# Optimization experiments

Hardware: AMD Instinct MI355X
Metric: run time of the kernel (lower is better)

Reference implementation:

```python
import jax, jax.numpy as jnp
import numpy as np

C = 128          # channels
L = 2            # num_layers
NA = 30000       # nodes of type 'a'
NB = 30000       # nodes of type 'b'
E = 150000       # edges per edge type
SEED_SIZE = 1024
EPS = 1e-5


def _ln(x, g, b):
    # LayerNorm over last dim (biased variance, eps=1e-5), matches nn.LayerNorm / PyG LayerNorm(mode='node')
    m = x.mean(-1, keepdims=True)
    v = ((x - m) ** 2).mean(-1, keepdims=True)
    return (x - m) * jax.lax.rsqrt(v + EPS) * g + b


def _seg_mean(msg, dst, n):
    # PyG aggr='mean': mean of incoming messages, 0 for isolated nodes
    s = jax.ops.segment_sum(msg, dst, num_segments=n)
    cnt = jax.ops.segment_sum(jnp.ones((dst.shape[0],), msg.dtype), dst, num_segments=n)
    return s / jnp.maximum(cnt, 1.0)[:, None]


def _prmp_conv(x_src, x_dst, edge, w1, b1, w2, b2, g, be, uw, ub):
    src, dst = edge[0], edge[1]
    xi = x_dst[dst]                                   # [E, C] dst feats per edge
    xj = x_src[src]                                   # [E, C] src feats per edge
    h = jax.nn.relu(jax.lax.stop_gradient(xi) @ w1 + b1)  # pred_mlp on detached x_i
    pred = h @ w2 + b2
    msg = _ln(xj - pred, g, be)                       # LayerNorm(residual) per edge
    agg = _seg_mean(msg, dst, x_dst.shape[0])         # mean aggregation to dst nodes
    return jax.nn.relu(jnp.concatenate([x_dst, agg], -1) @ uw + ub)  # update_mlp


def setup_inputs() -> dict:
    key = jax.random.key(0)
    ks = jax.random.split(key, 12)
    edge_ab = jnp.stack([jax.random.randint(ks[2], (E,), 0, NA, jnp.int32),
                         jax.random.randint(ks[3], (E,), 0, NB, jnp.int32)])
    edge_ba = jnp.stack([jax.random.randint(ks[4], (E,), 0, NB, jnp.int32),
                         jax.random.randint(ks[5], (E,), 0, NA, jnp.int32)])
    return {
        "x_a": jax.random.normal(ks[0], (NA, C), jnp.float32),
        "x_b": jax.random.normal(ks[1], (NB, C), jnp.float32),
        "edge_ab": edge_ab,
        "edge_ba": edge_ba,
        "pred_w1": jax.random.normal(ks[6], (L, 2, C, C), jnp.float32) * 0.05,
        "pred_b1": jnp.zeros((L, 2, C), jnp.float32),
        "pred_w2": jax.random.normal(ks[7], (L, 2, C, C), jnp.float32) * 0.05,
        "pred_b2": jnp.zeros((L, 2, C), jnp.float32),
        "msg_gamma": jnp.ones((L, 2, C), jnp.float32),
        "msg_beta": jnp.zeros((L, 2, C), jnp.float32),
        "upd_w": jax.random.normal(ks[8], (L, 2, 2 * C, C), jnp.float32) * 0.05,
        "upd_b": jnp.zeros((L, 2, C), jnp.float32),
        "node_gamma": jnp.ones((L, 2, C), jnp.float32),
        "node_beta": jnp.zeros((L, 2, C), jnp.float32),
        "head_w": jax.random.normal(ks[9], (C, 1), jnp.float32) * 0.05,
        "head_b": jnp.zeros((1,), jnp.float32),
        "seed_size": SEED_SIZE,
    }


def reference(x_a, x_b, edge_ab, edge_ba, pred_w1, pred_b1, pred_w2, pred_b2,
              msg_gamma, msg_beta, upd_w, upd_b, node_gamma, node_beta,
              head_w, head_b, seed_size):
    enc = lambda t: jnp.nan_to_num(t, nan=0.0, posinf=1.0, neginf=-1.0)
    x_a, x_b = enc(x_a), enc(x_b)
    for l in range(L):
        # edge type 0: a -> b ; edge type 1: b -> a (HeteroConv aggr='sum' is trivial: one conv per dst type)
        nb = _prmp_conv(x_a, x_b, edge_ab, pred_w1[l, 0], pred_b1[l, 0], pred_w2[l, 0], pred_b2[l, 0],
                        msg_gamma[l, 0], msg_beta[l, 0], upd_w[l, 0], upd_b[l, 0])
        na = _prmp_conv(x_b, x_a, edge_ba, pred_w1[l, 1], pred_b1[l, 1], pred_w2[l, 1], pred_b2[l, 1],
                        msg_gamma[l, 1], msg_beta[l, 1], upd_w[l, 1], upd_b[l, 1])
        na = jnp.nan_to_num(na, nan=0.0, posinf=10.0, neginf=-10.0)
        nb = jnp.nan_to_num(nb, nan=0.0, posinf=10.0, neginf=-10.0)
        x_a = jax.nn.relu(_ln(na, node_gamma[l, 0], node_beta[l, 0]))
        x_b = jax.nn.relu(_ln(nb, node_gamma[l, 1], node_beta[l, 1]))
    # head: single Linear(C -> 1) on the seed nodes of the entity table (type 'a')
    return x_a[:seed_size] @ head_w + head_b
```

## Files before the change

kernel.cpp:

```cpp
#include <hip/hip_runtime.h>

#define CC 128
#define SCAN_T 1024
#define SCAN_I 4

typedef __attribute__((ext_vector_type(8))) short bf16x8;
typedef __attribute__((ext_vector_type(4))) float f32x4;
#define MFMA16(a, b, c) __builtin_amdgcn_mfma_f32_16x16x32_bf16(a, b, c, 0, 0, 0)

__device__ __forceinline__ float enc_nan(float v) {
    if (v != v) return 0.f;
    if (v > 3.0e38f) return 1.f;
    if (v < -3.0e38f) return -1.f;
    return v;
}

__device__ __forceinline__ ushort f2bf(float x) {
    unsigned u = __builtin_bit_cast(unsigned, x);
    u += 0x7fff + ((u >> 16) & 1);
    return (ushort)(u >> 16);
}
__device__ __forceinline__ float bf2f(ushort h) {
    return __builtin_bit_cast(float, ((unsigned)h) << 16);
}

__device__ __forceinline__ int swz128(int row, int k) { return (row * 128 + k) ^ ((row & 7) << 3); }
__device__ __forceinline__ int swz256(int row, int k) { return (row * 256 + k) ^ ((row & 7) << 3); }

__global__ __launch_bounds__(256)
void k_init(const float* __restrict__ xin, ushort* __restrict__ xbf,
            float2* __restrict__ stat, int N)
{
    int row = blockIdx.x * 8 + (threadIdx.x >> 5);
    int s = threadIdx.x & 31;
    if (row >= N) return;
    float4 v = *reinterpret_cast<const float4*>(xin + (size_t)row * CC + s * 4);
    ushort h0 = f2bf(enc_nan(v.x)), h1 = f2bf(enc_nan(v.y));
    ushort h2 = f2bf(enc_nan(v.z)), h3 = f2bf(enc_nan(v.w));
    ushort4 hv = make_ushort4(h0, h1, h2, h3);
    *reinterpret_cast<ushort4*>(xbf + (size_t)row * CC + s * 4) = hv;
    float r0 = bf2f(h0), r1 = bf2f(h1), r2 = bf2f(h2), r3 = bf2f(h3);
    float sm = (r0 + r1) + (r2 + r3);
    float sq = fmaf(r0, r0, fmaf(r1, r1, fmaf(r2, r2, r3 * r3)));
    #pragma unroll
    for (int m = 1; m < 32; m <<= 1) { sm += __shfl_xor(sm, m); sq += __shfl_xor(sq, m); }
    if (s == 0) stat[row] = make_float2(sm, sq);
}

__global__ __launch_bounds__(256)
void k_wcvt(const float* __restrict__ pw1, const float* __restrict__ pw2,
            const float* __restrict__ uw,
            ushort* __restrict__ w1t, ushort* __restrict__ w2t, ushort* __restrict__ uwt)
{
    int i = blockIdx.x * 256 + threadIdx.x;
    int t = i >> 16;
    int r = i & 65535;
    if (r < 16384) {
        int k = r >> 7, c = r & 127;
        w1t[(size_t)t * 16384 + c * 128 + k] = f2bf(pw1[(size_t)t * 16384 + k * 128 + c]);
    } else if (r < 32768) {
        int rr = r - 16384;
        int k = rr >> 7, c = rr & 127;
        w2t[(size_t)t * 16384 + c * 128 + k] = f2bf(pw2[(size_t)t * 16384 + k * 128 + c]);
    } else {
        int rr = r - 32768;
        int k = rr >> 7, c = rr & 127;
        uwt[(size_t)t * 32768 + c * 256 + k] = f2bf(uw[(size_t)t * 32768 + k * 128 + c]);
    }
}

__global__ __launch_bounds__(256)
void k_hist_dual(const int* __restrict__ dst_b, int Eab, int* __restrict__ cnt_b,
                 const int* __restrict__ dst_a, int Eba, int* __restrict__ cnt_a)
{
    int i = blockIdx.x * 256 + threadIdx.x;
    if (i < Eab) atomicAdd(&cnt_b[dst_b[i]], 1);
    else if (i - Eab < Eba) atomicAdd(&cnt_a[dst_a[i - Eab]], 1);
}

__global__ __launch_bounds__(SCAN_T)
void k_scan_dual(const int* __restrict__ cnt0, int* __restrict__ rowp0, int* __restrict__ off0, int n0,
                 const int* __restrict__ cnt1, int* __restrict__ rowp1, int* __restrict__ off1, int n1)
{
    const int* cnt = (blockIdx.x == 0) ? cnt0 : cnt1;
    int* row_ptr   = (blockIdx.x == 0) ? rowp0 : rowp1;
    int* off       = (blockIdx.x == 0) ? off0 : off1;
    int n          = (blockIdx.x == 0) ? n0 : n1;

    __shared__ int wsum[SCAN_T / 64];
    __shared__ int carry_s;
    const int tid = threadIdx.x, lane = tid & 63, wid = tid >> 6;
    if (tid == 0) carry_s = 0;
    __syncthreads();
    const int chunk = SCAN_T * SCAN_I;
    for (int base = 0; base < n; base += chunk) {
        int i0 = base + tid * SCAN_I;
        int v[SCAN_I];
        int local = 0;
        #pragma unroll
        for (int t = 0; t < SCAN_I; ++t) {
            int i = i0 + t;
            v[t] = (i < n) ? cnt[i] : 0;
            local += v[t];
        }
        int incl = local;
        #pragma unroll
        for (int d = 1; d < 64; d <<= 1) {
            int t = __shfl_up(incl, d);
            if (lane >= d) incl += t;
        }
        if (lane == 63) wsum[wid] = incl;
        __syncthreads();
        if (wid == 0) {
            int wv = (lane < SCAN_T / 64) ? wsum[lane] : 0;
            int winc = wv;
            #pragma unroll
            for (int d = 1; d < SCAN_T / 64; d <<= 1) {
                int t = __shfl_up(winc, d);
                if (lane >= d) winc += t;
            }
            if (lane < SCAN_T / 64) wsum[lane] = winc - wv;
        }
        __syncthreads();
        int carry = carry_s;
        int excl = carry + wsum[wid] + incl - local;
        #pragma unroll
        for (int t = 0; t < SCAN_I; ++t) {
            int i = i0 + t;
            if (i < n) { row_ptr[i] = excl; off[i] = excl; }
            excl += v[t];
        }
        __syncthreads();
        if (tid == SCAN_T - 1) carry_s = carry + wsum[SCAN_T / 64 - 1] + incl;
        __syncthreads();
    }
    if (threadIdx.x == 0) row_ptr[n] = carry_s;
}

__global__ __launch_bounds__(256)
void k_scatter_dual(const int* __restrict__ src_b, const int* __restrict__ dst_b, int Eab,
                    int* __restrict__ off_b, int* __restrict__ srcs_ab,
                    const int* __restrict__ src_a, const int* __restrict__ dst_a, int Eba,
                    int* __restrict__ off_a, int* __restrict__ srcs_ba)
{
    int i = blockIdx.x * 256 + threadIdx.x;
    if (i < Eab) {
        int p = atomicAdd(&off_b[dst_b[i]], 1);
        srcs_ab[p] = src_b[i];
    } else if (i - Eab < Eba) {
        int j = i - Eab;
        int p = atomicAdd(&off_a[dst_a[j]], 1);
        srcs_ba[p] = src_a[j];
    }
}

__device__ __forceinline__ void pred_body(
    ushort* As, ushort* Hs,
    const ushort* __restrict__ xbf, ushort* __restrict__ pred_bf, int N, int blk,
    const ushort* __restrict__ w1t, const float* __restrict__ b1,
    const ushort* __restrict__ w2t, const float* __restrict__ b2)
{
    const int tid = threadIdx.x;
    const int base = blk * 32;

    {
        int row = tid >> 3, k0 = (tid & 7) << 4;
        int node = base + row;
        bf16x8 v0 = {}, v1 = {};
        if (node < N) {
            v0 = *reinterpret_cast<const bf16x8*>(xbf + (size_t)node * CC + k0);
            v1 = *reinterpret_cast<const bf16x8*>(xbf + (size_t)node * CC + k0 + 8);
        }
        *reinterpret_cast<bf16x8*>(&As[swz128(row, k0)])     = v0;
        *reinterpret_cast<bf16x8*>(&As[swz128(row, k0 + 8)]) = v1;
    }
    __syncthreads();

    const int w = tid >> 6, l = tid & 63;
    const int lr = l & 15, lg = l >> 4;

    f32x4 acc[2][2] = {};
    for (int kb = 0; kb < 4; ++kb) {
        int k = kb * 32 + lg * 8;
        bf16x8 a0 = *reinterpret_cast<const bf16x8*>(&As[swz128(lr, k)]);
        bf16x8 a1 = *reinterpret_cast<const bf16x8*>(&As[swz128(lr + 16, k)]);
        bf16x8 b0 = *reinterpret_cast<const bf16x8*>(&w1t[(size_t)(w * 32 + lr) * 128 + k]);
        bf16x8 b1v = *reinterpret_cast<const bf16x8*>(&w1t[(size_t)(w * 32 + 16 + lr) * 128 + k]);
        acc[0][0] = MFMA16(a0, b0, acc[0][0]);
        acc[0][1] = MFMA16(a0, b1v, acc[0][1]);
        acc[1][0] = MFMA16(a1, b0, acc[1][0]);
        acc[1][1] = MFMA16(a1, b1v, acc[1][1]);
    }
    {
        float bc[2] = { b1[w * 32 + lr], b1[w * 32 + 16 + lr] };
        #pragma unroll
        for (int mi = 0; mi < 2; ++mi)
            #pragma unroll
            for (int ni = 0; ni < 2; ++ni) {
                int col = w * 32 + ni * 16 + lr;
                #pragma unroll
                for (int j = 0; j < 4; ++j) {
                    int row = mi * 16 + lg * 4 + j;
                    Hs[swz128(row, col)] = f2bf(fmaxf(acc[mi][ni][j] + bc[ni], 0.f));
                }
            }
    }
    __syncthreads();

    f32x4 acc2[2][2] = {};
    for (int kb = 0; kb < 4; ++kb) {
        int k = kb * 32 + lg * 8;
        bf16x8 a0 = *reinterpret_cast<const bf16x8*>(&Hs[swz128(lr, k)]);
        bf16x8 a1 = *reinterpret_cast<const bf16x8*>(&Hs[swz128(lr + 16, k)]);
        bf16x8 b0 = *reinterpret_cast<const bf16x8*>(&w2t[(size_t)(w * 32 + lr) * 128 + k]);
        bf16x8 b1v = *reinterpret_cast<const bf16x8*>(&w2t[(size_t)(w * 32 + 16 + lr) * 128 + k]);
        acc2[0][0] = MFMA16(a0, b0, acc2[0][0]);
        acc2[0][1] = MFMA16(a0, b1v, acc2[0][1]);
        acc2[1][0] = MFMA16(a1, b0, acc2[1][0]);
        acc2[1][1] = MFMA16(a1, b1v, acc2[1][1]);
    }
    {
        float bc[2] = { b2[w * 32 + lr], b2[w * 32 + 16 + lr] };
        #pragma unroll
        for (int mi = 0; mi < 2; ++mi)
            #pragma unroll
            for (int ni = 0; ni < 2; ++ni) {
                int col = w * 32 + ni * 16 + lr;
                #pragma unroll
                for (int j = 0; j < 4; ++j) {
                    int row = mi * 16 + lg * 4 + j;
                    int node = base + row;
                    if (node < N)
                        pred_bf[(size_t)node * CC + col] = f2bf(acc2[mi][ni][j] + bc[ni]);
                }
            }
    }
}

__global__ __launch_bounds__(256)
void k_pred_dual(const ushort* __restrict__ xb, ushort* __restrict__ prd_b, int NB, int GB,
                 const ushort* __restrict__ w1t0, const float* __restrict__ b10,
                 const ushort* __restrict__ w2t0, const float* __restrict__ b20,
                 const ushort* __restrict__ xa, ushort* __restrict__ prd_a, int NA,
                 const ushort* __restrict__ w1t1, const float* __restrict__ b11,
                 const ushort* __restrict__ w2t1, const float* __restrict__ b21)
{
    __shared__ __align__(16) ushort As[32 * 128];
    __shared__ __align__(16) ushort Hs[32 * 128];
    if ((int)blockIdx.x < GB)
        pred_body(As, Hs, xb, prd_b, NB, blockIdx.x, w1t0, b10, w2t0, b20);
    else
        pred_body(As, Hs, xa, prd_a, NA, blockIdx.x - GB, w1t1, b11, w2t1, b21);
}

__device__ __forceinline__ void agg_body(
    const int* __restrict__ rowp, const int* __restrict__ srcs,
    const ushort* __restrict__ xsrc, const float2* __restrict__ statx,
    const ushort* __restrict__ pred_bf, const float* __restrict__ g,
    const float* __restrict__ be, ushort* __restrict__ agg_bf, int N, int blk)
{
    const int wid = threadIdx.x >> 6;
    const int lane = threadIdx.x & 63;
    const int d = blk * 4 + wid;
    if (d >= N) return;
    const int quarter = lane >> 4;
    const int c = (lane & 15) * 8;
    const int jb = rowp[d], je = rowp[d + 1];
    const int deg = je - jb;

    bf16x8 prb = *reinterpret_cast<const bf16x8*>(pred_bf + (size_t)d * CC + c);
    float pr[8];
    #pragma unroll
    for (int i = 0; i < 8; ++i) pr[i] = bf2f((ushort)prb[i]);

    float sp = 0.f, qp = 0.f;
    #pragma unroll
    for (int i = 0; i < 8; ++i) { sp += pr[i]; qp = fmaf(pr[i], pr[i], qp); }
    #pragma unroll
    for (int m = 1; m < 16; m <<= 1) { sp += __shfl_xor(sp, m); qp += __shfl_xor(qp, m); }

    float a[8] = {};
    float rsum = 0.f, cmsum = 0.f;
    for (int j = jb + quarter; j < je; j += 4) {
        const int sidx = srcs[j];
        bf16x8 xb_ = *reinterpret_cast<const bf16x8*>(xsrc + (size_t)sidx * CC + c);
        const float2 st = statx[sidx];
        float xj[8];
        #pragma unroll
        for (int i = 0; i < 8; ++i) xj[i] = bf2f((ushort)xb_[i]);
        float dot = 0.f;
        #pragma unroll
        for (int i = 0; i < 8; ++i) dot = fmaf(xj[i], pr[i], dot);
        #pragma unroll
        for (int m = 1; m < 16; m <<= 1) dot += __shfl_xor(dot, m);
        const float mean = (st.x - sp) * (1.f / 128.f);
        const float var = fmaf(-2.f, dot, st.y + qp) * (1.f / 128.f) - mean * mean;
        const float r = rsqrtf(var + 1e-5f);
        rsum += r;
        cmsum = fmaf(mean, r, cmsum);
        #pragma unroll
        for (int i = 0; i < 8; ++i) a[i] = fmaf(xj[i], r, a[i]);
    }
    #pragma unroll
    for (int i = 0; i < 8; ++i) { a[i] += __shfl_xor(a[i], 16); a[i] += __shfl_xor(a[i], 32); }
    rsum += __shfl_xor(rsum, 16);  rsum += __shfl_xor(rsum, 32);
    cmsum += __shfl_xor(cmsum, 16); cmsum += __shfl_xor(cmsum, 32);

    if (quarter == 0) {
        ushort o8[8];
        if (deg > 0) {
            const float inv = 1.f / (float)deg;
            const float4 g0 = *reinterpret_cast<const float4*>(g + c);
            const float4 g1 = *reinterpret_cast<const float4*>(g + c + 4);
            const float4 b0 = *reinterpret_cast<const float4*>(be + c);
            const float4 b1 = *reinterpret_cast<const float4*>(be + c + 4);
            const float gv[8] = { g0.x, g0.y, g0.z, g0.w, g1.x, g1.y, g1.z, g1.w };
            const float bv[8] = { b0.x, b0.y, b0.z, b0.w, b1.x, b1.y, b1.z, b1.w };
            #pragma unroll
            for (int i = 0; i < 8; ++i)
                o8[i] = f2bf(fmaf((a[i] - pr[i] * rsum - cmsum) * inv, gv[i], bv[i]));
        } else {
            #pragma unroll
            for (int i = 0; i < 8; ++i) o8[i] = 0;
        }
        *reinterpret_cast<bf16x8*>(agg_bf + (size_t)d * CC + c) =
            *reinterpret_cast<bf16x8*>(&o8[0]);
    }
}

__global__ __launch_bounds__(256)
void k_agg_dual(const int* __restrict__ rowp_b, const int* __restrict__ srcs_ab,
                const ushort* __restrict__ xa, const float2* __restrict__ stat_a,
                const ushort* __restrict__ prd_b, const float* __restrict__ g0,
                const float* __restrict__ be0, ushort* __restrict__ agg_b, int NB, int GBa,
                const int* __restrict__ rowp_a, const int* __restrict__ srcs_ba,
                const ushort* __restrict__ xb, const float2* __restrict__ stat_b,
                const ushort* __restrict__ prd_a, const float* __restrict__ g1,
                const float* __restrict__ be1, ushort* __restrict__ agg_a, int NA)
{
    if ((int)blockIdx.x < GBa)
        agg_body(rowp_b, srcs_ab, xa, stat_a, prd_b, g0, be0, agg_b, NB, blockIdx.x);
    else
        agg_body(rowp_a, srcs_ba, xb, stat_b, prd_a, g1, be1, agg_a, NA, blockIdx.x - GBa);
}

__device__ __forceinline__ void update_body(
    ushort* As, float (*os)[CC + 4],
    const ushort* __restrict__ xbf, const ushort* __restrict__ agg_bf,
    ushort* __restrict__ xout, float2* __restrict__ statOut, int N, int blk,
    const ushort* __restrict__ uwt, const float* __restrict__ ub,
    const float* __restrict__ ng, const float* __restrict__ nb,
    const float* __restrict__ hw, const float* __restrict__ hb,
    float* __restrict__ hout, int headS)
{
    const int tid = threadIdx.x;
    const int base = blk * 32;

    {
        int row = tid >> 3, k0 = (tid & 7) << 4;
        int node = base + row;
        bf16x8 v0 = {}, v1 = {}, v2 = {}, v3 = {};
        if (node < N) {
            v0 = *reinterpret_cast<const bf16x8*>(xbf + (size_t)node * CC + k0);
            v1 = *reinterpret_cast<const bf16x8*>(xbf + (size_t)node * CC + k0 + 8);
            v2 = *reinterpret_cast<const bf16x8*>(agg_bf + (size_t)node * CC + k0);
            v3 = *reinterpret_cast<const bf16x8*>(agg_bf + (size_t)node * CC + k0 + 8);
        }
        *reinterpret_cast<bf16x8*>(&As[swz256(row, k0)])           = v0;
        *reinterpret_cast<bf16x8*>(&As[swz256(row, k0 + 8)])       = v1;
        *reinterpret_cast<bf16x8*>(&As[swz256(row, 128 + k0)])     = v2;
        *reinterpret_cast<bf16x8*>(&As[swz256(row, 128 + k0 + 8)]) = v3;
    }
    __syncthreads();

    const int w = tid >> 6, l = tid & 63;
    const int lr = l & 15, lg = l >> 4;

    f32x4 acc[2][2] = {};
    for (int kb = 0; kb < 8; ++kb) {
        int k = kb * 32 + lg * 8;
        bf16x8 a0 = *reinterpret_cast<const bf16x8*>(&As[swz256(lr, k)]);
        bf16x8 a1 = *reinterpret_cast<const bf16x8*>(&As[swz256(lr + 16, k)]);
        bf16x8 b0 = *reinterpret_cast<const bf16x8*>(&uwt[(size_t)(w * 32 + lr) * 256 + k]);
        bf16x8 b1v = *reinterpret_cast<const bf16x8*>(&uwt[(size_t)(w * 32 + 16 + lr) * 256 + k]);
        acc[0][0] = MFMA16(a0, b0, acc[0][0]);
        acc[0][1] = MFMA16(a0, b1v, acc[0][1]);
        acc[1][0] = MFMA16(a1, b0, acc[1][0]);
        acc[1][1] = MFMA16(a1, b1v, acc[1][1]);
    }
    {
        float bc[2] = { ub[w * 32 + lr], ub[w * 32 + 16 + lr] };
        #pragma unroll
        for (int mi = 0; mi < 2; ++mi)
            #pragma unroll
            for (int ni = 0; ni < 2; ++ni) {
                int col = w * 32 + ni * 16 + lr;
                #pragma unroll
                for (int j = 0; j < 4; ++j) {
                    int row = mi * 16 + lg * 4 + j;
                    os[row][col] = fmaxf(acc[mi][ni][j] + bc[ni], 0.f);
                }
            }
    }
    __syncthreads();

    const int lane = tid & 63;
    const int nl = (tid >> 6) * 8 + (lane >> 3);
    const int cl = lane & 7;
    float vals[16];
    float sm = 0.f, sq = 0.f;
    #pragma unroll
    for (int t = 0; t < 16; ++t) {
        float u = os[nl][cl + 8 * t];
        vals[t] = u; sm += u; sq = fmaf(u, u, sq);
    }
    #pragma unroll
    for (int m = 1; m < 8; m <<= 1) { sm += __shfl_xor(sm, m); sq += __shfl_xor(sq, m); }
    float mean = sm * (1.f / 128.f);
    float var = sq * (1.f / 128.f) - mean * mean;
    float r = rsqrtf(var + 1e-5f);
    int node = base + nl;
    if (node < N) {
        float so = 0.f, sqo = 0.f, hsum = 0.f;
        bool doHead = (node < headS);
        #pragma unroll
        for (int t = 0; t < 16; ++t) {
            int cch = cl + 8 * t;
            float o = fmaxf(fmaf((vals[t] - mean) * r, ng[cch], nb[cch]), 0.f);
            ushort ob = f2bf(o);
            xout[(size_t)node * CC + cch] = ob;
            float orr = bf2f(ob);
            so += orr; sqo = fmaf(orr, orr, sqo);
            if (doHead) hsum = fmaf(o, hw[cch], hsum);
        }
        #pragma unroll
        for (int m = 1; m < 8; m <<= 1) { so += __shfl_xor(so, m); sqo += __shfl_xor(sqo, m); }
        if (doHead) {
            #pragma unroll
            for (int m = 1; m < 8; m <<= 1) hsum += __shfl_xor(hsum, m);
            if (cl == 0) hout[node] = hsum + hb[0];
        }
        if (cl == 0) statOut[node] = make_float2(so, sqo);
    }
}

__global__ __launch_bounds__(256)
void k_update_dual(const ushort* __restrict__ xb, const ushort* __restrict__ agg_b,
                   ushort* __restrict__ xb_o, float2* __restrict__ stat_b, int NB, int GB,
                   const ushort* __restrict__ uwt0, const float* __restrict__ ub0,
                   const float* __restrict__ ng0, const float* __restrict__ nb0,
                   const ushort* __restrict__ xa, const ushort* __restrict__ agg_a,
                   ushort* __restrict__ xa_o, float2* __restrict__ stat_a, int NA,
                   const ushort* __restrict__ uwt1, const float* __restrict__ ub1,
                   const float* __restrict__ ng1, const float* __restrict__ nb1,
                   const float* __restrict__ hw, const float* __restrict__ hb,
                   float* __restrict__ hout, int headS)
{
    __shared__ __align__(16) ushort As[32 * 256];
    __shared__ float os[32][CC + 4];
    if ((int)blockIdx.x < GB)
        update_body(As, os, xb, agg_b, xb_o, stat_b, NB, blockIdx.x,
                    uwt0, ub0, ng0, nb0, hw, hb, hout, 0);
    else
        update_body(As, os, xa, agg_a, xa_o, stat_a, NA, blockIdx.x - GB,
                    uwt1, ub1, ng1, nb1, hw, hb, hout, headS);
}

extern "C" void kernel_launch(void* const* d_in, const int* in_sizes, int n_in,
                              void* d_out, int out_size, void* d_ws, size_t ws_size,
                              hipStream_t stream)
{
    const float* x_a_in = (const float*)d_in[0];
    const float* x_b_in = (const float*)d_in[1];
    const int*   e_ab   = (const int*)d_in[2];
    const int*   e_ba   = (const int*)d_in[3];
    const float* pw1    = (const float*)d_in[4];
    const float* pb1    = (const float*)d_in[5];
    const float* pw2    = (const float*)d_in[6];
    const float* pb2    = (const float*)d_in[7];
    const float* mgam   = (const float*)d_in[8];
    const float* mbet   = (const float*)d_in[9];
    const float* uw     = (const float*)d_in[10];
    const float* ubias  = (const float*)d_in[11];
    const float* ngam   = (const float*)d_in[12];
    const float* nbet   = (const float*)d_in[13];
    const float* hw     = (const float*)d_in[14];
    const float* hb     = (const float*)d_in[15];

    const int NA  = in_sizes[0] / CC;
    const int NB  = in_sizes[1] / CC;
    const int Eab = in_sizes[2] / 2;
    const int Eba = in_sizes[3] / 2;

    float* ws = (float*)d_ws;
    size_t off = 0;
    ushort* xa    = (ushort*)(ws + off); off += (size_t)NA * CC / 2;
    ushort* xb    = (ushort*)(ws + off); off += (size_t)NB * CC / 2;
    ushort* prd_b = (ushort*)(ws + off); off += (size_t)NB * CC / 2;
    ushort* prd_a = (ushort*)(ws + off); off += (size_t)NA * CC / 2;
    ushort* agg_a = (ushort*)(ws + off); off += (size_t)NA * CC / 2;
    ushort* agg_b = (ushort*)(ws + off); off += (size_t)NB * CC / 2;
    float2* stat_a = (float2*)(ws + off); off += (size_t)NA * 2;
    float2* stat_b = (float2*)(ws + off); off += (size_t)NB * 2;
    ushort* w1t  = (ushort*)(ws + off); off += 4 * 16384 / 2;
    ushort* w2t  = (ushort*)(ws + off); off += 4 * 16384 / 2;
    ushort* uwt  = (ushort*)(ws + off); off += 4 * 32768 / 2;
    int* iw = (int*)(ws + off);
    size_t ioff = 0;
    int* cnt_b   = iw + ioff; ioff += NB;
    int* cnt_a   = iw + ioff; ioff += NA;
    int* rowp_b  = iw + ioff; ioff += NB + 1;
    int* rowp_a  = iw + ioff; ioff += NA + 1;
    int* off_b   = iw + ioff; ioff += NB;
    int* off_a   = iw + ioff; ioff += NA;
    int* srcs_ab = iw + ioff; ioff += Eab;
    int* srcs_ba = iw + ioff; ioff += Eba;

    const int GB  = (NB + 31) / 32, GA = (NA + 31) / 32;
    const int GBa = (NB + 3) / 4,  GAa = (NA + 3) / 4;

    k_init<<<dim3((NA + 7) / 8), dim3(256), 0, stream>>>(x_a_in, xa, stat_a, NA);
    k_init<<<dim3((NB + 7) / 8), dim3(256), 0, stream>>>(x_b_in, xb, stat_b, NB);

    k_wcvt<<<dim3(1024), dim3(256), 0, stream>>>(pw1, pw2, uw, w1t, w2t, uwt);

    hipMemsetAsync(cnt_b, 0, (size_t)(NB + NA) * sizeof(int), stream);
    k_hist_dual<<<dim3((Eab + Eba + 255) / 256), dim3(256), 0, stream>>>(
        e_ab + Eab, Eab, cnt_b, e_ba + Eba, Eba, cnt_a);
    k_scan_dual<<<dim3(2), dim3(SCAN_T), 0, stream>>>(
        cnt_b, rowp_b, off_b, NB, cnt_a, rowp_a, off_a, NA);
    k_scatter_dual<<<dim3((Eab + Eba + 255) / 256), dim3(256), 0, stream>>>(
        e_ab, e_ab + Eab, Eab, off_b, srcs_ab,
        e_ba, e_ba + Eba, Eba, off_a, srcs_ba);

    for (int l = 0; l < 2; ++l) {
        int t0 = l * 2 + 0;
        int t1 = l * 2 + 1;
        int headS = (l == 1) ? out_size : 0;

        k_pred_dual<<<dim3(GB + GA), dim3(256), 0, stream>>>(
            xb, prd_b, NB, GB,
            w1t + (size_t)t0 * 16384, pb1 + t0 * CC, w2t + (size_t)t0 * 16384, pb2 + t0 * CC,
            xa, prd_a, NA,
            w1t + (size_t)t1 * 16384, pb1 + t1 * CC, w2t + (size_t)t1 * 16384, pb2 + t1 * CC);

        k_agg_dual<<<dim3(GBa + GAa), dim3(256), 0, stream>>>(
            rowp_b, srcs_ab, xa, stat_a, prd_b, mgam + t0 * CC, mbet + t0 * CC, agg_b, NB, GBa,
            rowp_a, srcs_ba, xb, stat_b, prd_a, mgam + t1 * CC, mbet + t1 * CC, agg_a, NA);

        k_update_dual<<<dim3(GB + GA), dim3(256), 0, stream>>>(
            xb, agg_b, xb, stat_b, NB, GB,
            uwt + (size_t)t0 * 32768, ubias + t0 * CC, ngam + t0 * CC, nbet + t0 * CC,
            xa, agg_a, xa, stat_a, NA,
            uwt + (size_t)t1 * 32768, ubias + t1 * CC, ngam + t1 * CC, nbet + t1 * CC,
            hw, hb, (float*)d_out, headS);
    }
}
```

Measured before the change: 241.1 us.

## Fuse prediction MLP, edge aggregation and update MLP into one per-layer kernel

Replaces the three per-layer kernels (pred, agg, update) with a single kernel in which each 32-node block computes the prediction MLP into shared memory, aggregates neighbour messages into shared memory, then runs the update MLP and node LayerNorm. Node features and stats are now double-buffered across layers, and the two init launches are merged into one. This removes the global round-trips of the pred and agg intermediates and two launches per layer. In exchange, the aggregation now runs with one wave per 8 nodes in sequence inside the fused block, which may reduce latency hiding for the irregular gathers.

```diff
diff --git a/kernel.cpp b/kernel.cpp
--- a/kernel.cpp
+++ b/kernel.cpp
@@ -25,26 +25,32 @@
 }
 
 __device__ __forceinline__ int swz128(int row, int k) { return (row * 128 + k) ^ ((row & 7) << 3); }
-__device__ __forceinline__ int swz256(int row, int k) { return (row * 256 + k) ^ ((row & 7) << 3); }
 
 __global__ __launch_bounds__(256)
-void k_init(const float* __restrict__ xin, ushort* __restrict__ xbf,
-            float2* __restrict__ stat, int N)
+void k_init_dual(const float* __restrict__ xa_in, ushort* __restrict__ xa,
+                 float2* __restrict__ stat_a, int NA,
+                 const float* __restrict__ xb_in, ushort* __restrict__ xb,
+                 float2* __restrict__ stat_b, int NB)
 {
     int row = blockIdx.x * 8 + (threadIdx.x >> 5);
     int s = threadIdx.x & 31;
-    if (row >= N) return;
+    const float* xin; ushort* xo; float2* st;
+    if (row < NA) { xin = xa_in; xo = xa; st = stat_a; }
+    else {
+        row -= NA;
+        if (row >= NB) return;
+        xin = xb_in; xo = xb; st = stat_b;
+    }
     float4 v = *reinterpret_cast<const float4*>(xin + (size_t)row * CC + s * 4);
     ushort h0 = f2bf(enc_nan(v.x)), h1 = f2bf(enc_nan(v.y));
     ushort h2 = f2bf(enc_nan(v.z)), h3 = f2bf(enc_nan(v.w));
-    ushort4 hv = make_ushort4(h0, h1, h2, h3);
-    *reinterpret_cast<ushort4*>(xbf + (size_t)row * CC + s * 4) = hv;
+    *reinterpret_cast<ushort4*>(xo + (size_t)row * CC + s * 4) = make_ushort4(h0, h1, h2, h3);
     float r0 = bf2f(h0), r1 = bf2f(h1), r2 = bf2f(h2), r3 = bf2f(h3);
     float sm = (r0 + r1) + (r2 + r3);
     float sq = fmaf(r0, r0, fmaf(r1, r1, fmaf(r2, r2, r3 * r3)));
     #pragma unroll
     for (int m = 1; m < 32; m <<= 1) { sm += __shfl_xor(sm, m); sq += __shfl_xor(sq, m); }
-    if (s == 0) stat[row] = make_float2(sm, sq);
+    if (s == 0) st[row] = make_float2(sm, sq);
 }
 
 __global__ __launch_bounds__(256)
@@ -154,12 +160,25 @@
     }
 }
 
-__device__ __forceinline__ void pred_body(
-    ushort* As, ushort* Hs,
-    const ushort* __restrict__ xbf, ushort* __restrict__ pred_bf, int N, int blk,
+__device__ __forceinline__ void layer_body(
+    char* smem,
+    const ushort* __restrict__ xdst, const ushort* __restrict__ xsrc,
+    const float2* __restrict__ stat_src,
+    const int* __restrict__ rowp, const int* __restrict__ srcs,
     const ushort* __restrict__ w1t, const float* __restrict__ b1,
-    const ushort* __restrict__ w2t, const float* __restrict__ b2)
-{
+    const ushort* __restrict__ w2t, const float* __restrict__ b2,
+    const float* __restrict__ mg, const float* __restrict__ mbt,
+    const ushort* __restrict__ uwt, const float* __restrict__ ub,
+    const float* __restrict__ ng, const float* __restrict__ nb,
+    ushort* __restrict__ xout, float2* __restrict__ statOut, int N, int blk,
+    const float* __restrict__ hw, const float* __restrict__ hb,
+    float* __restrict__ hout, int headS)
+{
+    ushort* As = (ushort*)smem;
+    ushort* Hs = (ushort*)(smem + 8192);
+    ushort* P  = (ushort*)(smem + 16384);
+    float (*os)[CC + 4] = (float(*)[CC + 4])(smem + 8192);
+
     const int tid = threadIdx.x;
     const int base = blk * 32;
 
@@ -168,8 +187,8 @@
         int node = base + row;
         bf16x8 v0 = {}, v1 = {};
         if (node < N) {
-            v0 = *reinterpret_cast<const bf16x8*>(xbf + (size_t)node * CC + k0);
-            v1 = *reinterpret_cast<const bf16x8*>(xbf + (size_t)node * CC + k0 + 8);
+            v0 = *reinterpret_cast<const bf16x8*>(xdst + (size_t)node * CC + k0);
+            v1 = *reinterpret_cast<const bf16x8*>(xdst + (size_t)node * CC + k0 + 8);
         }
         *reinterpret_cast<bf16x8*>(&As[swz128(row, k0)])     = v0;
         *reinterpret_cast<bf16x8*>(&As[swz128(row, k0 + 8)]) = v1;
@@ -179,19 +198,19 @@
     const int w = tid >> 6, l = tid & 63;
     const int lr = l & 15, lg = l >> 4;
 
-    f32x4 acc[2][2] = {};
-    for (int kb = 0; kb < 4; ++kb) {
-        int k = kb * 32 + lg * 8;
-        bf16x8 a0 = *reinterpret_cast<const bf16x8*>(&As[swz128(lr, k)]);
-        bf16x8 a1 = *reinterpret_cast<const bf16x8*>(&As[swz128(lr + 16, k)]);
-        bf16x8 b0 = *reinterpret_cast<const bf16x8*>(&w1t[(size_t)(w * 32 + lr) * 128 + k]);
-        bf16x8 b1v = *reinterpret_cast<const bf16x8*>(&w1t[(size_t)(w * 32 + 16 + lr) * 128 + k]);
-        acc[0][0] = MFMA16(a0, b0, acc[0][0]);
-        acc[0][1] = MFMA16(a0, b1v, acc[0][1]);
-        acc[1][0] = MFMA16(a1, b0, acc[1][0]);
-        acc[1][1] = MFMA16(a1, b1v, acc[1][1]);
-    }
     {
+        f32x4 acc[2][2] = {};
+        for (int kb = 0; kb < 4; ++kb) {
+            int k = kb * 32 + lg * 8;
+            bf16x8 a0 = *reinterpret_cast<const bf16x8*>(&As[swz128(lr, k)]);
+            bf16x8 a1 = *reinterpret_cast<const bf16x8*>(&As[swz128(lr + 16, k)]);
+            bf16x8 b0 = *reinterpret_cast<const bf16x8*>(&w1t[(size_t)(w * 32 + lr) * 128 + k]);
+            bf16x8 b1v = *reinterpret_cast<const bf16x8*>(&w1t[(size_t)(w * 32 + 16 + lr) * 128 + k]);
+            acc[0][0] = MFMA16(a0, b0, acc[0][0]);
+            acc[0][1] = MFMA16(a0, b1v, acc[0][1]);
+            acc[1][0] = MFMA16(a1, b0, acc[1][0]);
+            acc[1][1] = MFMA16(a1, b1v, acc[1][1]);
+        }
         float bc[2] = { b1[w * 32 + lr], b1[w * 32 + 16 + lr] };
         #pragma unroll
         for (int mi = 0; mi < 2; ++mi)
@@ -207,19 +226,19 @@
     }
     __syncthreads();
 
-    f32x4 acc2[2][2] = {};
-    for (int kb = 0; kb < 4; ++kb) {
-        int k = kb * 32 + lg * 8;
-        bf16x8 a0 = *reinterpret_cast<const bf16x8*>(&Hs[swz128(lr, k)]);
-        bf16x8 a1 = *reinterpret_cast<const bf16x8*>(&Hs[swz128(lr + 16, k)]);
-        bf16x8 b0 = *reinterpret_cast<const bf16x8*>(&w2t[(size_t)(w * 32 + lr) * 128 + k]);
-        bf16x8 b1v = *reinterpret_cast<const bf16x8*>(&w2t[(size_t)(w * 32 + 16 + lr) * 128 + k]);
-        acc2[0][0] = MFMA16(a0, b0, acc2[0][0]);
-        acc2[0][1] = MFMA16(a0, b1v, acc2[0][1]);
-        acc2[1][0] = MFMA16(a1, b0, acc2[1][0]);
-        acc2[1][1] = MFMA16(a1, b1v, acc2[1][1]);
-    }
     {
+        f32x4 acc[2][2] = {};
+        for (int kb = 0; kb < 4; ++kb) {
+            int k = kb * 32 + lg * 8;
+            bf16x8 a0 = *reinterpret_cast<const bf16x8*>(&Hs[swz128(lr, k)]);
+            bf16x8 a1 = *reinterpret_cast<const bf16x8*>(&Hs[swz128(lr + 16, k)]);
+            bf16x8 b0 = *reinterpret_cast<const bf16x8*>(&w2t[(size_t)(w * 32 + lr) * 128 + k]);
+            bf16x8 b1v = *reinterpret_cast<const bf16x8*>(&w2t[(size_t)(w * 32 + 16 + lr) * 128 + k]);
+            acc[0][0] = MFMA16(a0, b0, acc[0][0]);
+            acc[0][1] = MFMA16(a0, b1v, acc[0][1]);
+            acc[1][0] = MFMA16(a1, b0, acc[1][0]);
+            acc[1][1] = MFMA16(a1, b1v, acc[1][1]);
+        }
         float bc[2] = { b2[w * 32 + lr], b2[w * 32 + 16 + lr] };
         #pragma unroll
         for (int mi = 0; mi < 2; ++mi)
@@ -229,158 +248,86 @@
                 #pragma unroll
                 for (int j = 0; j < 4; ++j) {
                     int row = mi * 16 + lg * 4 + j;
-                    int node = base + row;
-                    if (node < N)
-                        pred_bf[(size_t)node * CC + col] = f2bf(acc2[mi][ni][j] + bc[ni]);
+                    P[row * CC + col] = f2bf(acc[mi][ni][j] + bc[ni]);
                 }
             }
     }
-}
-
-__global__ __launch_bounds__(256)
-void k_pred_dual(const ushort* __restrict__ xb, ushort* __restrict__ prd_b, int NB, int GB,
-                 const ushort* __restrict__ w1t0, const float* __restrict__ b10,
-                 const ushort* __restrict__ w2t0, const float* __restrict__ b20,
-                 const ushort* __restrict__ xa, ushort* __restrict__ prd_a, int NA,
-                 const ushort* __restrict__ w1t1, const float* __restrict__ b11,
-                 const ushort* __restrict__ w2t1, const float* __restrict__ b21)
-{
-    __shared__ __align__(16) ushort As[32 * 128];
-    __shared__ __align__(16) ushort Hs[32 * 128];
-    if ((int)blockIdx.x < GB)
-        pred_body(As, Hs, xb, prd_b, NB, blockIdx.x, w1t0, b10, w2t0, b20);
-    else
-        pred_body(As, Hs, xa, prd_a, NA, blockIdx.x - GB, w1t1, b11, w2t1, b21);
-}
-
-__device__ __forceinline__ void agg_body(
-    const int* __restrict__ rowp, const int* __restrict__ srcs,
-    const ushort* __restrict__ xsrc, const float2* __restrict__ statx,
-    const ushort* __restrict__ pred_bf, const float* __restrict__ g,
-    const float* __restrict__ be, ushort* __restrict__ agg_bf, int N, int blk)
-{
-    const int wid = threadIdx.x >> 6;
-    const int lane = threadIdx.x & 63;
-    const int d = blk * 4 + wid;
-    if (d >= N) return;
-    const int quarter = lane >> 4;
-    const int c = (lane & 15) * 8;
-    const int jb = rowp[d], je = rowp[d + 1];
-    const int deg = je - jb;
-
-    bf16x8 prb = *reinterpret_cast<const bf16x8*>(pred_bf + (size_t)d * CC + c);
-    float pr[8];
-    #pragma unroll
-    for (int i = 0; i < 8; ++i) pr[i] = bf2f((ushort)prb[i]);
-
-    float sp = 0.f, qp = 0.f;
-    #pragma unroll
-    for (int i = 0; i < 8; ++i) { sp += pr[i]; qp = fmaf(pr[i], pr[i], qp); }
-    #pragma unroll
-    for (int m = 1; m < 16; m <<= 1) { sp += __shfl_xor(sp, m); qp += __shfl_xor(qp, m); }
-
-    float a[8] = {};
-    float rsum = 0.f, cmsum = 0.f;
-    for (int j = jb + quarter; j < je; j += 4) {
-        const int sidx = srcs[j];
-        bf16x8 xb_ = *reinterpret_cast<const bf16x8*>(xsrc + (size_t)sidx * CC + c);
-        const float2 st = statx[sidx];
-        float xj[8];
-        #pragma unroll
-        for (int i = 0; i < 8; ++i) xj[i] = bf2f((ushort)xb_[i]);
-        float dot = 0.f;
-        #pragma unroll
-        for (int i = 0; i < 8; ++i) dot = fmaf(xj[i], pr[i], dot);
-        #pragma unroll
-        for (int m = 1; m < 16; m <<= 1) dot += __shfl_xor(dot, m);
-        const float mean = (st.x - sp) * (1.f / 128.f);
-        const float var = fmaf(-2.f, dot, st.y + qp) * (1.f / 128.f) - mean * mean;
-        const float r = rsqrtf(var + 1e-5f);
-        rsum += r;
-        cmsum = fmaf(mean, r, cmsum);
-        #pragma unroll
-        for (int i = 0; i < 8; ++i) a[i] = fmaf(xj[i], r, a[i]);
-    }
-    #pragma unroll
-    for (int i = 0; i < 8; ++i) { a[i] += __shfl_xor(a[i], 16); a[i] += __shfl_xor(a[i], 32); }
-    rsum += __shfl_xor(rsum, 16);  rsum += __shfl_xor(rsum, 32);
-    cmsum += __shfl_xor(cmsum, 16); cmsum += __shfl_xor(cmsum, 32);
-
-    if (quarter == 0) {
-        ushort o8[8];
-        if (deg > 0) {
-            const float inv = 1.f / (float)deg;
-            const float4 g0 = *reinterpret_cast<const float4*>(g + c);
-            const float4 g1 = *reinterpret_cast<const float4*>(g + c + 4);
-            const float4 b0 = *reinterpret_cast<const float4*>(be + c);
-            const float4 b1 = *reinterpret_cast<const float4*>(be + c + 4);
-            const float gv[8] = { g0.x, g0.y, g0.z, g0.w, g1.x, g1.y, g1.z, g1.w };
-            const float bv[8] = { b0.x, b0.y, b0.z, b0.w, b1.x, b1.y, b1.z, b1.w };
-            #pragma unroll
-            for (int i = 0; i < 8; ++i)
-                o8[i] = f2bf(fmaf((a[i] - pr[i] * rsum - cmsum) * inv, gv[i], bv[i]));
-        } else {
-            #pragma unroll
-            for (int i = 0; i < 8; ++i) o8[i] = 0;
-        }
-        *reinterpret_cast<bf16x8*>(agg_bf + (size_t)d * CC + c) =
-            *reinterpret_cast<bf16x8*>(&o8[0]);
-    }
-}
-
-__global__ __launch_bounds__(256)
-void k_agg_dual(const int* __restrict__ rowp_b, const int* __restrict__ srcs_ab,
-                const ushort* __restrict__ xa, const float2* __restrict__ stat_a,
-                const ushort* __restrict__ prd_b, const float* __restrict__ g0,
-                const float* __restrict__ be0, ushort* __restrict__ agg_b, int NB, int GBa,
-                const int* __restrict__ rowp_a, const int* __restrict__ srcs_ba,
-                const ushort* __restrict__ xb, const float2* __restrict__ stat_b,
-                const ushort* __restrict__ prd_a, const float* __restrict__ g1,
-                const float* __restrict__ be1, ushort* __restrict__ agg_a, int NA)
-{
-    if ((int)blockIdx.x < GBa)
-        agg_body(rowp_b, srcs_ab, xa, stat_a, prd_b, g0, be0, agg_b, NB, blockIdx.x);
-    else
-        agg_body(rowp_a, srcs_ba, xb, stat_b, prd_a, g1, be1, agg_a, NA, blockIdx.x - GBa);
-}
-
-__device__ __forceinline__ void update_body(
-    ushort* As, float (*os)[CC + 4],
-    const ushort* __restrict__ xbf, const ushort* __restrict__ agg_bf,
-    ushort* __restrict__ xout, float2* __restrict__ statOut, int N, int blk,
-    const ushort* __restrict__ uwt, const float* __restrict__ ub,
-    const float* __restrict__ ng, const float* __restrict__ nb,
-    const float* __restrict__ hw, const float* __restrict__ hb,
-    float* __restrict__ hout, int headS)
-{
-    const int tid = threadIdx.x;
-    const int base = blk * 32;
+    __syncthreads();
 
     {
-        int row = tid >> 3, k0 = (tid & 7) << 4;
-        int node = base + row;
-        bf16x8 v0 = {}, v1 = {}, v2 = {}, v3 = {};
-        if (node < N) {
-            v0 = *reinterpret_cast<const bf16x8*>(xbf + (size_t)node * CC + k0);
-            v1 = *reinterpret_cast<const bf16x8*>(xbf + (size_t)node * CC + k0 + 8);
-            v2 = *reinterpret_cast<const bf16x8*>(agg_bf + (size_t)node * CC + k0);
-            v3 = *reinterpret_cast<const bf16x8*>(agg_bf + (size_t)node * CC + k0 + 8);
-        }
-        *reinterpret_cast<bf16x8*>(&As[swz256(row, k0)])           = v0;
-        *reinterpret_cast<bf16x8*>(&As[swz256(row, k0 + 8)])       = v1;
-        *reinterpret_cast<bf16x8*>(&As[swz256(row, 128 + k0)])     = v2;
-        *reinterpret_cast<bf16x8*>(&As[swz256(row, 128 + k0 + 8)]) = v3;
-    }
-    __syncthreads();
-
-    const int w = tid >> 6, l = tid & 63;
-    const int lr = l & 15, lg = l >> 4;
+        const int quarter = l >> 4;
+        const int c = (l & 15) * 8;
+        const float4 g0 = *reinterpret_cast<const float4*>(mg + c);
+        const float4 g1 = *reinterpret_cast<const float4*>(mg + c + 4);
+        const float4 e0 = *reinterpret_cast<const float4*>(mbt + c);
+        const float4 e1 = *reinterpret_cast<const float4*>(mbt + c + 4);
+        const float gv[8] = { g0.x, g0.y, g0.z, g0.w, g1.x, g1.y, g1.z, g1.w };
+        const float bv[8] = { e0.x, e0.y, e0.z, e0.w, e1.x, e1.y, e1.z, e1.w };
+        for (int i = 0; i < 8; ++i) {
+            const int nl_ = w * 8 + i;
+            const int d = base + nl_;
+            if (d >= N) break;
+            bf16x8 prb = *reinterpret_cast<const bf16x8*>(&P[nl_ * CC + c]);
+            float pr[8];
+            #pragma unroll
+            for (int q = 0; q < 8; ++q) pr[q] = bf2f((ushort)prb[q]);
+            float sp = 0.f, qp = 0.f;
+            #pragma unroll
+            for (int q = 0; q < 8; ++q) { sp += pr[q]; qp = fmaf(pr[q], pr[q], qp); }
+            #pragma unroll
+            for (int m = 1; m < 16; m <<= 1) { sp += __shfl_xor(sp, m); qp += __shfl_xor(qp, m); }
+            const int jb = rowp[d], je = rowp[d + 1];
+            const int deg = je - jb;
+            float a[8] = {};
+            float rsum = 0.f, cmsum = 0.f;
+            for (int j = jb + quarter; j < je; j += 4) {
+                const int sidx = srcs[j];
+                bf16x8 xb_ = *reinterpret_cast<const bf16x8*>(xsrc + (size_t)sidx * CC + c);
+                const float2 st = stat_src[sidx];
+                float xj[8];
+                #pragma unroll
+                for (int q = 0; q < 8; ++q) xj[q] = bf2f((ushort)xb_[q]);
+                float dot = 0.f;
+                #pragma unroll
+                for (int q = 0; q < 8; ++q) dot = fmaf(xj[q], pr[q], dot);
+                #pragma unroll
+                for (int m = 1; m < 16; m <<= 1) dot += __shfl_xor(dot, m);
+                const float mean = (st.x - sp) * (1.f / 128.f);
+                const float var = fmaf(-2.f, dot, st.y + qp) * (1.f / 128.f) - mean * mean;
+                const float r = rsqrtf(var + 1e-5f);
+                rsum += r;
+                cmsum = fmaf(mean, r, cmsum);
+                #pragma unroll
+                for (int q = 0; q < 8; ++q) a[q] = fmaf(xj[q], r, a[q]);
+            }
+            #pragma unroll
+            for (int q = 0; q < 8; ++q) { a[q] += __shfl_xor(a[q], 16); a[q] += __shfl_xor(a[q], 32); }
+            rsum += __shfl_xor(rsum, 16);  rsum += __shfl_xor(rsum, 32);
+            cmsum += __shfl_xor(cmsum, 16); cmsum += __shfl_xor(cmsum, 32);
+            if (quarter == 0) {
+                ushort o8[8];
+                if (deg > 0) {
+                    const float inv = 1.f / (float)deg;
+                    #pragma unroll
+                    for (int q = 0; q < 8; ++q)
+                        o8[q] = f2bf(fmaf((a[q] - pr[q] * rsum - cmsum) * inv, gv[q], bv[q]));
+                } else {
+                    #pragma unroll
+                    for (int q = 0; q < 8; ++q) o8[q] = 0;
+                }
+                *reinterpret_cast<bf16x8*>(&Hs[swz128(nl_, c)]) = *reinterpret_cast<bf16x8*>(&o8[0]);
+            }
+        }
+    }
+    __syncthreads();
 
     f32x4 acc[2][2] = {};
     for (int kb = 0; kb < 8; ++kb) {
         int k = kb * 32 + lg * 8;
-        bf16x8 a0 = *reinterpret_cast<const bf16x8*>(&As[swz256(lr, k)]);
-        bf16x8 a1 = *reinterpret_cast<const bf16x8*>(&As[swz256(lr + 16, k)]);
+        const ushort* Ab = (k < 128) ? As : Hs;
+        int kl = k & 127;
+        bf16x8 a0 = *reinterpret_cast<const bf16x8*>(&Ab[swz128(lr, kl)]);
+        bf16x8 a1 = *reinterpret_cast<const bf16x8*>(&Ab[swz128(lr + 16, kl)]);
         bf16x8 b0 = *reinterpret_cast<const bf16x8*>(&uwt[(size_t)(w * 32 + lr) * 256 + k]);
         bf16x8 b1v = *reinterpret_cast<const bf16x8*>(&uwt[(size_t)(w * 32 + 16 + lr) * 256 + k]);
         acc[0][0] = MFMA16(a0, b0, acc[0][0]);
@@ -388,6 +335,8 @@
         acc[1][0] = MFMA16(a1, b0, acc[1][0]);
         acc[1][1] = MFMA16(a1, b1v, acc[1][1]);
     }
+    __syncthreads();
+
     {
         float bc[2] = { ub[w * 32 + lr], ub[w * 32 + 16 + lr] };
         #pragma unroll
@@ -404,9 +353,8 @@
     }
     __syncthreads();
 
-    const int lane = tid & 63;
-    const int nl = (tid >> 6) * 8 + (lane >> 3);
-    const int cl = lane & 7;
+    const int nl = w * 8 + (l >> 3);
+    const int cl = l & 7;
     float vals[16];
     float sm = 0.f, sq = 0.f;
     #pragma unroll
@@ -445,25 +393,36 @@
 }
 
 __global__ __launch_bounds__(256)
-void k_update_dual(const ushort* __restrict__ xb, const ushort* __restrict__ agg_b,
-                   ushort* __restrict__ xb_o, float2* __restrict__ stat_b, int NB, int GB,
-                   const ushort* __restrict__ uwt0, const float* __restrict__ ub0,
-                   const float* __restrict__ ng0, const float* __restrict__ nb0,
-                   const ushort* __restrict__ xa, const ushort* __restrict__ agg_a,
-                   ushort* __restrict__ xa_o, float2* __restrict__ stat_a, int NA,
-                   const ushort* __restrict__ uwt1, const float* __restrict__ ub1,
-                   const float* __restrict__ ng1, const float* __restrict__ nb1,
-                   const float* __restrict__ hw, const float* __restrict__ hb,
-                   float* __restrict__ hout, int headS)
-{
-    __shared__ __align__(16) ushort As[32 * 256];
-    __shared__ float os[32][CC + 4];
+void k_layer_dual(
+    const ushort* __restrict__ xb_c, const ushort* __restrict__ xa_c,
+    const float2* __restrict__ stat_a_c, const float2* __restrict__ stat_b_c,
+    const int* __restrict__ rowp_b, const int* __restrict__ srcs_ab,
+    const int* __restrict__ rowp_a, const int* __restrict__ srcs_ba,
+    ushort* __restrict__ xb_n, ushort* __restrict__ xa_n,
+    float2* __restrict__ stat_b_n, float2* __restrict__ stat_a_n,
+    int NB, int NA, int GB,
+    const ushort* __restrict__ w1t0, const float* __restrict__ b10,
+    const ushort* __restrict__ w2t0, const float* __restrict__ b20,
+    const float* __restrict__ mg0, const float* __restrict__ mb0,
+    const ushort* __restrict__ uwt0, const float* __restrict__ ub0,
+    const float* __restrict__ ng0, const float* __restrict__ nb0,
+    const ushort* __restrict__ w1t1, const float* __restrict__ b11,
+    const ushort* __restrict__ w2t1, const float* __restrict__ b21,
+    const float* __restrict__ mg1, const float* __restrict__ mb1,
+    const ushort* __restrict__ uwt1, const float* __restrict__ ub1,
+    const float* __restrict__ ng1, const float* __restrict__ nb1,
+    const float* __restrict__ hw, const float* __restrict__ hb,
+    float* __restrict__ hout, int headS)
+{
+    __shared__ __align__(16) char smem[25088];
     if ((int)blockIdx.x < GB)
-        update_body(As, os, xb, agg_b, xb_o, stat_b, NB, blockIdx.x,
-                    uwt0, ub0, ng0, nb0, hw, hb, hout, 0);
+        layer_body(smem, xb_c, xa_c, stat_a_c, rowp_b, srcs_ab,
+                   w1t0, b10, w2t0, b20, mg0, mb0, uwt0, ub0, ng0, nb0,
+                   xb_n, stat_b_n, NB, blockIdx.x, hw, hb, hout, 0);
     else
-        update_body(As, os, xa, agg_a, xa_o, stat_a, NA, blockIdx.x - GB,
-                    uwt1, ub1, ng1, nb1, hw, hb, hout, headS);
+        layer_body(smem, xa_c, xb_c, stat_b_c, rowp_a, srcs_ba,
+                   w1t1, b11, w2t1, b21, mg1, mb1, uwt1, ub1, ng1, nb1,
+                   xa_n, stat_a_n, NA, blockIdx.x - GB, hw, hb, hout, headS);
 }
 
 extern "C" void kernel_launch(void* const* d_in, const int* in_sizes, int n_in,
@@ -494,17 +453,17 @@
 
     float* ws = (float*)d_ws;
     size_t off = 0;
-    ushort* xa    = (ushort*)(ws + off); off += (size_t)NA * CC / 2;
-    ushort* xb    = (ushort*)(ws + off); off += (size_t)NB * CC / 2;
-    ushort* prd_b = (ushort*)(ws + off); off += (size_t)NB * CC / 2;
-    ushort* prd_a = (ushort*)(ws + off); off += (size_t)NA * CC / 2;
-    ushort* agg_a = (ushort*)(ws + off); off += (size_t)NA * CC / 2;
-    ushort* agg_b = (ushort*)(ws + off); off += (size_t)NB * CC / 2;
-    float2* stat_a = (float2*)(ws + off); off += (size_t)NA * 2;
-    float2* stat_b = (float2*)(ws + off); off += (size_t)NB * 2;
-    ushort* w1t  = (ushort*)(ws + off); off += 4 * 16384 / 2;
-    ushort* w2t  = (ushort*)(ws + off); off += 4 * 16384 / 2;
-    ushort* uwt  = (ushort*)(ws + off); off += 4 * 32768 / 2;
+    ushort* xa0 = (ushort*)(ws + off); off += (size_t)NA * CC / 2;
+    ushort* xa1 = (ushort*)(ws + off); off += (size_t)NA * CC / 2;
+    ushort* xb0 = (ushort*)(ws + off); off += (size_t)NB * CC / 2;
+    ushort* xb1 = (ushort*)(ws + off); off += (size_t)NB * CC / 2;
+    float2* sa0 = (float2*)(ws + off); off += (size_t)NA * 2;
+    float2* sa1 = (float2*)(ws + off); off += (size_t)NA * 2;
+    float2* sb0 = (float2*)(ws + off); off += (size_t)NB * 2;
+    float2* sb1 = (float2*)(ws + off); off += (size_t)NB * 2;
+    ushort* w1t = (ushort*)(ws + off); off += 4 * 16384 / 2;
+    ushort* w2t = (ushort*)(ws + off); off += 4 * 16384 / 2;
+    ushort* uwt = (ushort*)(ws + off); off += 4 * 32768 / 2;
     int* iw = (int*)(ws + off);
     size_t ioff = 0;
     int* cnt_b   = iw + ioff; ioff += NB;
@@ -516,11 +475,10 @@
     int* srcs_ab = iw + ioff; ioff += Eab;
     int* srcs_ba = iw + ioff; ioff += Eba;
 
-    const int GB  = (NB + 31) / 32, GA = (NA + 31) / 32;
-    const int GBa = (NB + 3) / 4,  GAa = (NA + 3) / 4;
-
-    k_init<<<dim3((NA + 7) / 8), dim3(256), 0, stream>>>(x_a_in, xa, stat_a, NA);
-    k_init<<<dim3((NB + 7) / 8), dim3(256), 0, stream>>>(x_b_in, xb, stat_b, NB);
+    const int GB = (NB + 31) / 32, GA = (NA + 31) / 32;
+
+    k_init_dual<<<dim3((NA + NB + 7) / 8), dim3(256), 0, stream>>>(
+        x_a_in, xa0, sa0, NA, x_b_in, xb0, sb0, NB);
 
     k_wcvt<<<dim3(1024), dim3(256), 0, stream>>>(pw1, pw2, uw, w1t, w2t, uwt);
 
@@ -533,26 +491,34 @@
         e_ab, e_ab + Eab, Eab, off_b, srcs_ab,
         e_ba, e_ba + Eba, Eba, off_a, srcs_ba);
 
-    for (int l = 0; l < 2; ++l) {
-        int t0 = l * 2 + 0;
-        int t1 = l * 2 + 1;
-        int headS = (l == 1) ? out_size : 0;
-
-        k_pred_dual<<<dim3(GB + GA), dim3(256), 0, stream>>>(
-            xb, prd_b, NB, GB,
+    ushort* xac = xa0; ushort* xan = xa1;
+    ushort* xbc = xb0; ushort* xbn = xb1;
+    float2* sac = sa0; float2* san = sa1;
+    float2* sbc = sb0; float2* sbn = sb1;
+
+    for (int lyr = 0; lyr < 2; ++lyr) {
+        int t0 = lyr * 2 + 0;
+        int t1 = lyr * 2 + 1;
+        int headS = (lyr == 1) ? out_size : 0;
+
+        k_layer_dual<<<dim3(GB + GA), dim3(256), 0, stream>>>(
+            xbc, xac, sac, sbc,
+            rowp_b, srcs_ab, rowp_a, srcs_ba,
+            xbn, xan, sbn, san,
+            NB, NA, GB,
             w1t + (size_t)t0 * 16384, pb1 + t0 * CC, w2t + (size_t)t0 * 16384, pb2 + t0 * CC,
-            xa, prd_a, NA,
-            w1t + (size_t)t1 * 16384, pb1 + t1 * CC, w2t + (size_t)t1 * 16384, pb2 + t1 * CC);
-
-        k_agg_dual<<<dim3(GBa + GAa), dim3(256), 0, stream>>>(
-            rowp_b, srcs_ab, xa, stat_a, prd_b, mgam + t0 * CC, mbet + t0 * CC, agg_b, NB, GBa,
-            rowp_a, srcs_ba, xb, stat_b, prd_a, mgam + t1 * CC, mbet + t1 * CC, agg_a, NA);
-
-        k_update_dual<<<dim3(GB + GA), dim3(256), 0, stream>>>(
-            xb, agg_b, xb, stat_b, NB, GB,
+            mgam + t0 * CC, mbet + t0 * CC,
             uwt + (size_t)t0 * 32768, ubias + t0 * CC, ngam + t0 * CC, nbet + t0 * CC,
-            xa, agg_a, xa, stat_a, NA,
+            w1t + (size_t)t1 * 16384, pb1 + t1 * CC, w2t + (size_t)t1 * 16384, pb2 + t1 * CC,
+            mgam + t1 * CC, mbet + t1 * CC,
             uwt + (size_t)t1 * 32768, ubias + t1 * CC, ngam + t1 * CC, nbet + t1 * CC,
             hw, hb, (float*)d_out, headS);
-    }
-}
+
+        ushort* t;
+        t = xac; xac = xan; xan = t;
+        t = xbc; xbc = xbn; xbn = t;
+        float2* s;
+        s = sac; sac = san; san = s;
+        s = sbc; sbc = sbn; sbn = s;
+    }
+}
```

After: 228.3 us. 5.3% less time.
